# Performance work log

Measured on AMD Instinct MI355X. Metric: run time of the kernel, lower is better.

Reference implementation:

```python
import jax, jax.numpy as jnp
import numpy as np

DIM = 1024
HEADS = 8
NUM_EXPERTS = 65536
NUM_KEYS = 256  # sqrt(NUM_EXPERTS)
DIM_KEY = 512
TOPK = 16  # product_key_topk == num_experts_per_head


def setup_inputs() -> dict:
    key = jax.random.key(0)
    ks = jax.random.split(key, 6)
    B, N = 2, 512
    x = jax.random.normal(ks[0], (B, N, DIM), dtype=jnp.float32)
    gamma = jnp.ones((DIM,), dtype=jnp.float32)
    wq = jax.random.normal(ks[1], (2 * HEADS * DIM_KEY, DIM), dtype=jnp.float32) * 0.02
    keys = jax.random.normal(ks[2], (HEADS, NUM_KEYS, 2, DIM_KEY), dtype=jnp.float32) * 0.02
    table_down = jax.random.normal(ks[3], (NUM_EXPERTS, DIM), dtype=jnp.float32) * 0.02
    table_up = jax.random.normal(ks[4], (NUM_EXPERTS, DIM), dtype=jnp.float32) * 0.02
    return {"x": x, "gamma": gamma, "wq": wq, "keys": keys,
            "table_down": table_down, "table_up": table_up}


def _rmsnorm(v, g):
    # torch F.normalize(x, dim=-1) * gamma * sqrt(dim)
    scale = jnp.sqrt(jnp.asarray(v.shape[-1], v.dtype))
    n = jnp.maximum(jnp.linalg.norm(v, axis=-1, keepdims=True), 1e-12)
    return v / n * g * scale


def reference(x, gamma, wq, keys, table_down, table_up):
    B, N, D = x.shape
    xn = _rmsnorm(x, gamma)          # pre_rmsnorm on x
    gate = xn                        # x_in_gate is None -> gate = norm(x)
    # queries: b n (p h d) -> p b n h d
    q = gate @ wq.T                  # [B,N,2*H*DK]
    q = q.reshape(B, N, 2, HEADS, DIM_KEY).transpose(2, 0, 1, 3, 4)  # [2,B,N,H,DK]
    # sim: p b n h d, h k p d -> p b n h k
    sim = jnp.einsum('pbnhd,hkpd->pbnhk', q, keys)
    sx, ix = jax.lax.top_k(sim[0], TOPK)  # [B,N,H,TOPK]
    sy, iy = jax.lax.top_k(sim[1], TOPK)
    # outer sums over the two product-key axes -> [B,N,H,TOPK*TOPK]
    all_scores = (sx[..., :, None] + sy[..., None, :]).reshape(B, N, HEADS, TOPK * TOPK)
    all_indices = (ix[..., :, None] * NUM_KEYS + iy[..., None, :]).reshape(B, N, HEADS, TOPK * TOPK)
    scores, pk = jax.lax.top_k(all_scores, TOPK)           # [B,N,H,K]
    indices = jnp.take_along_axis(all_indices, pk, axis=-1)  # expert ids [B,N,H,K]
    wd = table_down[indices]  # [B,N,H,K,D]
    wu = table_up[indices]    # [B,N,H,K,D]
    h = jnp.einsum('bnd,bnhkd->bnhk', xn, wd)
    h = jax.nn.gelu(h, approximate=False) * jax.nn.softmax(scores, axis=-1)
    out = jnp.einsum('bnhk,bnhkd->bnd', h, wu)
    return out
```

## Files before the change

kernel.cpp:

```cpp
#include <hip/hip_runtime.h>
#include <math.h>


#define DIMV 1024

__global__ __launch_bounds__(256) void peer_rmsnorm(const float* __restrict__ x,
                                                    const float* __restrict__ gamma,
                                                    float* __restrict__ xnf)
{
    int t = blockIdx.x;
    int tid = threadIdx.x;
    const float4* xr = (const float4*)(x + (size_t)t * DIMV);
    float4 v = xr[tid];
    double ss = (double)v.x*v.x + (double)v.y*v.y + (double)v.z*v.z + (double)v.w*v.w;
    #pragma unroll
    for (int off = 32; off > 0; off >>= 1) ss += __shfl_xor(ss, off);
    __shared__ double red[4];
    if ((tid & 63) == 0) red[tid >> 6] = ss;
    __syncthreads();
    double tot = red[0] + red[1] + red[2] + red[3];
    float n32 = (float)fmax(sqrt(tot), 1e-12);
    const float4* g4 = (const float4*)gamma;
    float4 gv = g4[tid];
    float4 o;
    o.x = __fmul_rn(__fmul_rn(__fdiv_rn(v.x, n32), gv.x), 32.0f);
    o.y = __fmul_rn(__fmul_rn(__fdiv_rn(v.y, n32), gv.y), 32.0f);
    o.z = __fmul_rn(__fmul_rn(__fdiv_rn(v.z, n32), gv.z), 32.0f);
    o.w = __fmul_rn(__fmul_rn(__fdiv_rn(v.w, n32), gv.w), 32.0f);
    ((float4*)(xnf + (size_t)t * DIMV))[tid] = o;
}

__global__ __launch_bounds__(128) void peer_qgemm(const float* __restrict__ A,
                                                  const float* __restrict__ Bm,
                                                  float* __restrict__ C)
{
    __shared__ float As[2][16][128];
    __shared__ float Bs[2][16][128];
    int tid = threadIdx.x;
    int m0 = blockIdx.y * 128, n0 = blockIdx.x * 128;
    int tx = tid & 15, ty = tid >> 4;
    float acc[16][8] = {};
    float4 av0 = *(const float4*)(A  + (long)(m0 + tid) * 1024 + 0);
    float4 av1 = *(const float4*)(A  + (long)(m0 + tid) * 1024 + 4);
    float4 av2 = *(const float4*)(A  + (long)(m0 + tid) * 1024 + 8);
    float4 av3 = *(const float4*)(A  + (long)(m0 + tid) * 1024 + 12);
    float4 bv0 = *(const float4*)(Bm + (long)(n0 + tid) * 1024 + 0);
    float4 bv1 = *(const float4*)(Bm + (long)(n0 + tid) * 1024 + 4);
    float4 bv2 = *(const float4*)(Bm + (long)(n0 + tid) * 1024 + 8);
    float4 bv3 = *(const float4*)(Bm + (long)(n0 + tid) * 1024 + 12);
    #pragma unroll
    for (int j = 0; j < 4; j++) {
        As[0][j][tid]      = ((const float*)&av0)[j];
        As[0][4 + j][tid]  = ((const float*)&av1)[j];
        As[0][8 + j][tid]  = ((const float*)&av2)[j];
        As[0][12 + j][tid] = ((const float*)&av3)[j];
        Bs[0][j][tid]      = ((const float*)&bv0)[j];
        Bs[0][4 + j][tid]  = ((const float*)&bv1)[j];
        Bs[0][8 + j][tid]  = ((const float*)&bv2)[j];
        Bs[0][12 + j][tid] = ((const float*)&bv3)[j];
    }
    __syncthreads();
    int cur = 0;
    for (int k0 = 0; k0 < 1024; k0 += 16) {
        bool more = (k0 + 16) < 1024;
        if (more) {
            av0 = *(const float4*)(A  + (long)(m0 + tid) * 1024 + (k0 + 16));
            av1 = *(const float4*)(A  + (long)(m0 + tid) * 1024 + (k0 + 20));
            av2 = *(const float4*)(A  + (long)(m0 + tid) * 1024 + (k0 + 24));
            av3 = *(const float4*)(A  + (long)(m0 + tid) * 1024 + (k0 + 28));
            bv0 = *(const float4*)(Bm + (long)(n0 + tid) * 1024 + (k0 + 16));
            bv1 = *(const float4*)(Bm + (long)(n0 + tid) * 1024 + (k0 + 20));
            bv2 = *(const float4*)(Bm + (long)(n0 + tid) * 1024 + (k0 + 24));
            bv3 = *(const float4*)(Bm + (long)(n0 + tid) * 1024 + (k0 + 28));
        }
        #pragma unroll
        for (int kk = 0; kk < 16; kk++) {
            float4 a0 = *(const float4*)&As[cur][kk][ty * 16];
            float4 a1 = *(const float4*)&As[cur][kk][ty * 16 + 4];
            float4 a2 = *(const float4*)&As[cur][kk][ty * 16 + 8];
            float4 a3 = *(const float4*)&As[cur][kk][ty * 16 + 12];
            float4 b0 = *(const float4*)&Bs[cur][kk][tx * 4];
            float4 b1 = *(const float4*)&Bs[cur][kk][tx * 4 + 64];
            float ra16[16] = {a0.x,a0.y,a0.z,a0.w, a1.x,a1.y,a1.z,a1.w,
                              a2.x,a2.y,a2.z,a2.w, a3.x,a3.y,a3.z,a3.w};
            float rb8[8]   = {b0.x,b0.y,b0.z,b0.w, b1.x,b1.y,b1.z,b1.w};
            #pragma unroll
            for (int i = 0; i < 16; i++)
                #pragma unroll
                for (int j = 0; j < 8; j++)
                    acc[i][j] = __fmaf_rn(ra16[i], rb8[j], acc[i][j]);
        }
        if (more) {
            int nxt = cur ^ 1;
            #pragma unroll
            for (int j = 0; j < 4; j++) {
                As[nxt][j][tid]      = ((const float*)&av0)[j];
                As[nxt][4 + j][tid]  = ((const float*)&av1)[j];
                As[nxt][8 + j][tid]  = ((const float*)&av2)[j];
                As[nxt][12 + j][tid] = ((const float*)&av3)[j];
                Bs[nxt][j][tid]      = ((const float*)&bv0)[j];
                Bs[nxt][4 + j][tid]  = ((const float*)&bv1)[j];
                Bs[nxt][8 + j][tid]  = ((const float*)&bv2)[j];
                Bs[nxt][12 + j][tid] = ((const float*)&bv3)[j];
            }
            __syncthreads();
            cur = nxt;
        }
    }
    #pragma unroll
    for (int i = 0; i < 16; i++) {
        float4 c0 = {acc[i][0], acc[i][1], acc[i][2], acc[i][3]};
        float4 c1 = {acc[i][4], acc[i][5], acc[i][6], acc[i][7]};
        long r = (long)(m0 + ty * 16 + i) * 8192 + n0;
        *(float4*)(C + r + tx * 4)      = c0;
        *(float4*)(C + r + 64 + tx * 4) = c1;
    }
}

__global__ __launch_bounds__(256) void peer_sim(const float* __restrict__ qf,
                                                const float* __restrict__ keys,
                                                float* __restrict__ simf)
{
    int tb = blockIdx.x;
    int z  = blockIdx.y;
    int h = z & 7, p = z >> 3;
    int tid = threadIdx.x;
    __shared__ float4 qs[16][128];
    int t0 = tb * 16;
    long qbase = (long)h * 512 + (long)p * 4096;
    int row = tid >> 4, c0 = (tid & 15) * 8;
    const float4* qrow = (const float4*)(qf + (long)(t0 + row) * 8192 + qbase);
    #pragma unroll
    for (int u = 0; u < 8; u++) qs[row][c0 + u] = qrow[c0 + u];
    __syncthreads();
    int k = tid;
    const float4* krow = (const float4*)(keys + (long)h * 262144 + (long)k * 1024 + (long)p * 512);
    float pa[16][4] = {};
    for (int d4 = 0; d4 < 128; d4++) {
        float4 kv = krow[d4];
        #pragma unroll
        for (int tt = 0; tt < 16; tt++) {
            float4 qv = qs[tt][d4];
            pa[tt][0] = __fadd_rn(pa[tt][0], __fmul_rn(qv.x, kv.x));
            pa[tt][1] = __fadd_rn(pa[tt][1], __fmul_rn(qv.y, kv.y));
            pa[tt][2] = __fadd_rn(pa[tt][2], __fmul_rn(qv.z, kv.z));
            pa[tt][3] = __fadd_rn(pa[tt][3], __fmul_rn(qv.w, kv.w));
        }
    }
    #pragma unroll
    for (int tt = 0; tt < 16; tt++) {
        float s = __fadd_rn(__fadd_rn(pa[tt][0], pa[tt][2]),
                            __fadd_rn(pa[tt][1], pa[tt][3]));
        simf[(long)(t0 + tt) * 4096 + (long)p * 2048 + h * 256 + k] = s;
    }
}

__device__ inline void peer_select16(float v[4], int lane, float* outv, int* outi)
{
    for (int iter = 0; iter < 16; iter++) {
        float bv = -INFINITY; int bk = 1 << 30;
        #pragma unroll
        for (int i = 0; i < 4; i++) {
            int k = i * 64 + lane;
            if (v[i] > bv || (v[i] == bv && k < bk)) { bv = v[i]; bk = k; }
        }
        #pragma unroll
        for (int off = 32; off > 0; off >>= 1) {
            float ov = __shfl_xor(bv, off);
            int   ok = __shfl_xor(bk, off);
            if (ov > bv || (ov == bv && ok < bk)) { bv = ov; bk = ok; }
        }
        if (lane == 0) { outv[iter] = bv; outi[iter] = bk; }
        __syncthreads();
        if ((bk & 63) == lane) v[bk >> 6] = -INFINITY;
    }
}

__global__ __launch_bounds__(64) void peer_topk(const float* __restrict__ sim,
                                                float* __restrict__ wsel,
                                                int* __restrict__ esel)
{
    int b = blockIdx.x;
    int t = b >> 3, h = b & 7;
    int lane = threadIdx.x;
    const float* simx = sim + (size_t)t * 4096 + h * 256;
    const float* simy = simx + 2048;
    __shared__ float sxv[16]; __shared__ int sxi[16];
    __shared__ float syv[16]; __shared__ int syi[16];
    __shared__ float cv[16];  __shared__ int cf[16];
    float v[4];
    #pragma unroll
    for (int i = 0; i < 4; i++) v[i] = simx[i*64 + lane];
    peer_select16(v, lane, sxv, sxi);
    __syncthreads();
    #pragma unroll
    for (int i = 0; i < 4; i++) v[i] = simy[i*64 + lane];
    peer_select16(v, lane, syv, syi);
    __syncthreads();
    #pragma unroll
    for (int i = 0; i < 4; i++) {
        int f = i*64 + lane;
        v[i] = __fadd_rn(sxv[f >> 4], syv[f & 15]);
    }
    peer_select16(v, lane, cv, cf);
    __syncthreads();
    double m = (double)cv[0];
    double w = (lane < 16) ? exp((double)cv[lane] - m) : 0.0;
    double Z = w;
    #pragma unroll
    for (int off = 32; off > 0; off >>= 1) Z += __shfl_xor(Z, off);
    if (lane < 16) {
        int f = cf[lane];
        esel[b * 16 + lane] = sxi[f >> 4] * 256 + syi[f & 15];
        wsel[b * 16 + lane] = (float)(w / Z);
    }
}

__global__ __launch_bounds__(256) void peer_downup(const float* __restrict__ xn,
                                                   const float* __restrict__ table_down,
                                                   const float* __restrict__ table_up,
                                                   const int* __restrict__ esel,
                                                   const float* __restrict__ wsel,
                                                   float* __restrict__ out)
{
    int t = blockIdx.x;
    int tid = threadIdx.x;
    int wid = tid >> 6, lane = tid & 63;
    __shared__ float4 xs[256];
    __shared__ float  gs[128];
    __shared__ int    es[128];
    if (tid < 128) es[tid] = esel[t * 128 + tid];
    xs[tid] = ((const float4*)(xn + (size_t)t * DIMV))[tid];
    __syncthreads();
    #pragma unroll 4
    for (int jj = 0; jj < 32; jj++) {
        int j = wid * 32 + jj;
        const float4* dr = (const float4*)(table_down + (size_t)es[j] * DIMV);
        double acc = 0.0;
        #pragma unroll
        for (int it = 0; it < 4; it++) {
            int d4 = it * 64 + lane;
            float4 a = xs[d4];
            float4 bb = dr[d4];
            acc = fma((double)a.x, (double)bb.x, acc);
            acc = fma((double)a.y, (double)bb.y, acc);
            acc = fma((double)a.z, (double)bb.z, acc);
            acc = fma((double)a.w, (double)bb.w, acc);
        }
        #pragma unroll
        for (int off = 32; off > 0; off >>= 1) acc += __shfl_xor(acc, off);
        if (lane == 0) {
            double hv = acc;
            double ge = 0.5 * hv * (1.0 + erf(hv * 0.70710678118654752));
            gs[j] = (float)(ge * (double)wsel[t * 128 + j]);
        }
    }
    __syncthreads();
    int dbase = tid * 4;
    double a0 = 0, a1 = 0, a2 = 0, a3 = 0;
    #pragma unroll 8
    for (int j = 0; j < 128; j++) {
        const float4 u = *(const float4*)(table_up + (size_t)es[j] * DIMV + dbase);
        double gj = (double)gs[j];
        a0 = fma(gj, (double)u.x, a0); a1 = fma(gj, (double)u.y, a1);
        a2 = fma(gj, (double)u.z, a2); a3 = fma(gj, (double)u.w, a3);
    }
    float4 o = {(float)a0, (float)a1, (float)a2, (float)a3};
    *(float4*)(out + (size_t)t * DIMV + dbase) = o;
}

extern "C" void kernel_launch(void* const* d_in, const int* in_sizes, int n_in,
                              void* d_out, int out_size, void* d_ws, size_t ws_size,
                              hipStream_t stream)
{
    const float* x          = (const float*)d_in[0];
    const float* gamma      = (const float*)d_in[1];
    const float* wq         = (const float*)d_in[2];
    const float* keys       = (const float*)d_in[3];
    const float* table_down = (const float*)d_in[4];
    const float* table_up   = (const float*)d_in[5];
    float* out = (float*)d_out;
    char* wsb  = (char*)d_ws;

    float* xnf  = (float*)(wsb);
    float* qf   = (float*)(wsb + (4ull<<20));
    float* simf = (float*)(wsb + (36ull<<20));
    float* wsel = (float*)(wsb + (52ull<<20));
    int*   esel = (int*)  (wsb + (52ull<<20) + (512ull<<10));
    if (ws_size < (54ull << 20)) return;

    peer_rmsnorm<<<1024, 256, 0, stream>>>(x, gamma, xnf);

    peer_qgemm<<<dim3(64, 8, 1), 128, 0, stream>>>(xnf, wq, qf);

    peer_sim<<<dim3(64, 16, 1), 256, 0, stream>>>(qf, keys, simf);

    peer_topk<<<8192, 64, 0, stream>>>(simf, wsel, esel);

    peer_downup<<<1024, 256, 0, stream>>>(xnf, table_down, table_up,
                                          esel, wsel, out);
}
```

Before: 559.8 us.

## Shrink query GEMM tile to 128x64 and software-prefetch gathered table rows

The query GEMM tile drops from 128x128 to 128x64, doubling the grid to 1024 blocks. Each thread now holds an 8x8 accumulator instead of 16x8, which cuts register pressure and improves occupancy on the 256-CU GPU. In the down/up gather kernel, the next expert's table_down row and the next four table_up rows are loaded into registers before the current ones are used. This overlaps gather latency with the FP64 FMAs, at the cost of extra registers.

```diff
diff --git a/kernel.cpp b/kernel.cpp
--- a/kernel.cpp
+++ b/kernel.cpp
@@ -35,29 +35,26 @@
                                                   float* __restrict__ C)
 {
     __shared__ float As[2][16][128];
-    __shared__ float Bs[2][16][128];
+    __shared__ float Bs[2][16][64];
     int tid = threadIdx.x;
-    int m0 = blockIdx.y * 128, n0 = blockIdx.x * 128;
-    int tx = tid & 15, ty = tid >> 4;
-    float acc[16][8] = {};
+    int n0 = blockIdx.x * 64, m0 = blockIdx.y * 128;
+    int tx = tid & 7, ty = tid >> 3;
+    int rb = tid >> 1, lk8 = (tid & 1) * 8;
+    float acc[8][8] = {};
     float4 av0 = *(const float4*)(A  + (long)(m0 + tid) * 1024 + 0);
     float4 av1 = *(const float4*)(A  + (long)(m0 + tid) * 1024 + 4);
     float4 av2 = *(const float4*)(A  + (long)(m0 + tid) * 1024 + 8);
     float4 av3 = *(const float4*)(A  + (long)(m0 + tid) * 1024 + 12);
-    float4 bv0 = *(const float4*)(Bm + (long)(n0 + tid) * 1024 + 0);
-    float4 bv1 = *(const float4*)(Bm + (long)(n0 + tid) * 1024 + 4);
-    float4 bv2 = *(const float4*)(Bm + (long)(n0 + tid) * 1024 + 8);
-    float4 bv3 = *(const float4*)(Bm + (long)(n0 + tid) * 1024 + 12);
+    float4 bv0 = *(const float4*)(Bm + (long)(n0 + rb) * 1024 + lk8);
+    float4 bv1 = *(const float4*)(Bm + (long)(n0 + rb) * 1024 + lk8 + 4);
     #pragma unroll
     for (int j = 0; j < 4; j++) {
         As[0][j][tid]      = ((const float*)&av0)[j];
         As[0][4 + j][tid]  = ((const float*)&av1)[j];
         As[0][8 + j][tid]  = ((const float*)&av2)[j];
         As[0][12 + j][tid] = ((const float*)&av3)[j];
-        Bs[0][j][tid]      = ((const float*)&bv0)[j];
-        Bs[0][4 + j][tid]  = ((const float*)&bv1)[j];
-        Bs[0][8 + j][tid]  = ((const float*)&bv2)[j];
-        Bs[0][12 + j][tid] = ((const float*)&bv3)[j];
+        Bs[0][lk8 + j][rb]     = ((const float*)&bv0)[j];
+        Bs[0][lk8 + 4 + j][rb] = ((const float*)&bv1)[j];
     }
     __syncthreads();
     int cur = 0;
@@ -68,27 +65,22 @@
             av1 = *(const float4*)(A  + (long)(m0 + tid) * 1024 + (k0 + 20));
             av2 = *(const float4*)(A  + (long)(m0 + tid) * 1024 + (k0 + 24));
             av3 = *(const float4*)(A  + (long)(m0 + tid) * 1024 + (k0 + 28));
-            bv0 = *(const float4*)(Bm + (long)(n0 + tid) * 1024 + (k0 + 16));
-            bv1 = *(const float4*)(Bm + (long)(n0 + tid) * 1024 + (k0 + 20));
-            bv2 = *(const float4*)(Bm + (long)(n0 + tid) * 1024 + (k0 + 24));
-            bv3 = *(const float4*)(Bm + (long)(n0 + tid) * 1024 + (k0 + 28));
+            bv0 = *(const float4*)(Bm + (long)(n0 + rb) * 1024 + (k0 + 16 + lk8));
+            bv1 = *(const float4*)(Bm + (long)(n0 + rb) * 1024 + (k0 + 20 + lk8));
         }
         #pragma unroll
         for (int kk = 0; kk < 16; kk++) {
-            float4 a0 = *(const float4*)&As[cur][kk][ty * 16];
-            float4 a1 = *(const float4*)&As[cur][kk][ty * 16 + 4];
-            float4 a2 = *(const float4*)&As[cur][kk][ty * 16 + 8];
-            float4 a3 = *(const float4*)&As[cur][kk][ty * 16 + 12];
-            float4 b0 = *(const float4*)&Bs[cur][kk][tx * 4];
-            float4 b1 = *(const float4*)&Bs[cur][kk][tx * 4 + 64];
-            float ra16[16] = {a0.x,a0.y,a0.z,a0.w, a1.x,a1.y,a1.z,a1.w,
-                              a2.x,a2.y,a2.z,a2.w, a3.x,a3.y,a3.z,a3.w};
-            float rb8[8]   = {b0.x,b0.y,b0.z,b0.w, b1.x,b1.y,b1.z,b1.w};
+            float4 a0 = *(const float4*)&As[cur][kk][ty * 8];
+            float4 a1 = *(const float4*)&As[cur][kk][ty * 8 + 4];
+            float4 b0 = *(const float4*)&Bs[cur][kk][tx * 8];
+            float4 b1 = *(const float4*)&Bs[cur][kk][tx * 8 + 4];
+            float ra8[8] = {a0.x,a0.y,a0.z,a0.w, a1.x,a1.y,a1.z,a1.w};
+            float rb8[8] = {b0.x,b0.y,b0.z,b0.w, b1.x,b1.y,b1.z,b1.w};
             #pragma unroll
-            for (int i = 0; i < 16; i++)
+            for (int i = 0; i < 8; i++)
                 #pragma unroll
                 for (int j = 0; j < 8; j++)
-                    acc[i][j] = __fmaf_rn(ra16[i], rb8[j], acc[i][j]);
+                    acc[i][j] = __fmaf_rn(ra8[i], rb8[j], acc[i][j]);
         }
         if (more) {
             int nxt = cur ^ 1;
@@ -98,22 +90,20 @@
                 As[nxt][4 + j][tid]  = ((const float*)&av1)[j];
                 As[nxt][8 + j][tid]  = ((const float*)&av2)[j];
                 As[nxt][12 + j][tid] = ((const float*)&av3)[j];
-                Bs[nxt][j][tid]      = ((const float*)&bv0)[j];
-                Bs[nxt][4 + j][tid]  = ((const float*)&bv1)[j];
-                Bs[nxt][8 + j][tid]  = ((const float*)&bv2)[j];
-                Bs[nxt][12 + j][tid] = ((const float*)&bv3)[j];
+                Bs[nxt][lk8 + j][rb]     = ((const float*)&bv0)[j];
+                Bs[nxt][lk8 + 4 + j][rb] = ((const float*)&bv1)[j];
             }
             __syncthreads();
             cur = nxt;
         }
     }
     #pragma unroll
-    for (int i = 0; i < 16; i++) {
+    for (int i = 0; i < 8; i++) {
         float4 c0 = {acc[i][0], acc[i][1], acc[i][2], acc[i][3]};
         float4 c1 = {acc[i][4], acc[i][5], acc[i][6], acc[i][7]};
-        long r = (long)(m0 + ty * 16 + i) * 8192 + n0;
-        *(float4*)(C + r + tx * 4)      = c0;
-        *(float4*)(C + r + 64 + tx * 4) = c1;
+        long r = (long)(m0 + ty * 8 + i) * 8192 + (n0 + tx * 8);
+        *(float4*)(C + r)     = c0;
+        *(float4*)(C + r + 4) = c1;
     }
 }
 
@@ -232,40 +222,68 @@
     if (tid < 128) es[tid] = esel[t * 128 + tid];
     xs[tid] = ((const float4*)(xn + (size_t)t * DIMV))[tid];
     __syncthreads();
-    #pragma unroll 4
+    int base = wid * 32;
+    const float4* dr = (const float4*)(table_down + (size_t)es[base] * DIMV);
+    float4 p0 = dr[lane], p1 = dr[64 + lane], p2 = dr[128 + lane], p3 = dr[192 + lane];
+    float4 a0 = xs[lane], a1 = xs[64 + lane], a2 = xs[128 + lane], a3 = xs[192 + lane];
     for (int jj = 0; jj < 32; jj++) {
-        int j = wid * 32 + jj;
-        const float4* dr = (const float4*)(table_down + (size_t)es[j] * DIMV);
+        float4 c0 = p0, c1 = p1, c2 = p2, c3 = p3;
+        if (jj < 31) {
+            const float4* nr = (const float4*)(table_down + (size_t)es[base + jj + 1] * DIMV);
+            p0 = nr[lane]; p1 = nr[64 + lane]; p2 = nr[128 + lane]; p3 = nr[192 + lane];
+        }
         double acc = 0.0;
-        #pragma unroll
-        for (int it = 0; it < 4; it++) {
-            int d4 = it * 64 + lane;
-            float4 a = xs[d4];
-            float4 bb = dr[d4];
-            acc = fma((double)a.x, (double)bb.x, acc);
-            acc = fma((double)a.y, (double)bb.y, acc);
-            acc = fma((double)a.z, (double)bb.z, acc);
-            acc = fma((double)a.w, (double)bb.w, acc);
-        }
+        acc = fma((double)a0.x, (double)c0.x, acc);
+        acc = fma((double)a0.y, (double)c0.y, acc);
+        acc = fma((double)a0.z, (double)c0.z, acc);
+        acc = fma((double)a0.w, (double)c0.w, acc);
+        acc = fma((double)a1.x, (double)c1.x, acc);
+        acc = fma((double)a1.y, (double)c1.y, acc);
+        acc = fma((double)a1.z, (double)c1.z, acc);
+        acc = fma((double)a1.w, (double)c1.w, acc);
+        acc = fma((double)a2.x, (double)c2.x, acc);
+        acc = fma((double)a2.y, (double)c2.y, acc);
+        acc = fma((double)a2.z, (double)c2.z, acc);
+        acc = fma((double)a2.w, (double)c2.w, acc);
+        acc = fma((double)a3.x, (double)c3.x, acc);
+        acc = fma((double)a3.y, (double)c3.y, acc);
+        acc = fma((double)a3.z, (double)c3.z, acc);
+        acc = fma((double)a3.w, (double)c3.w, acc);
         #pragma unroll
         for (int off = 32; off > 0; off >>= 1) acc += __shfl_xor(acc, off);
         if (lane == 0) {
             double hv = acc;
             double ge = 0.5 * hv * (1.0 + erf(hv * 0.70710678118654752));
-            gs[j] = (float)(ge * (double)wsel[t * 128 + j]);
+            gs[base + jj] = (float)(ge * (double)wsel[t * 128 + base + jj]);
         }
     }
     __syncthreads();
     int dbase = tid * 4;
-    double a0 = 0, a1 = 0, a2 = 0, a3 = 0;
-    #pragma unroll 8
-    for (int j = 0; j < 128; j++) {
-        const float4 u = *(const float4*)(table_up + (size_t)es[j] * DIMV + dbase);
-        double gj = (double)gs[j];
-        a0 = fma(gj, (double)u.x, a0); a1 = fma(gj, (double)u.y, a1);
-        a2 = fma(gj, (double)u.z, a2); a3 = fma(gj, (double)u.w, a3);
-    }
-    float4 o = {(float)a0, (float)a1, (float)a2, (float)a3};
+    double b0 = 0, b1 = 0, b2 = 0, b3 = 0;
+    float4 u0 = *(const float4*)(table_up + (size_t)es[0] * DIMV + dbase);
+    float4 u1 = *(const float4*)(table_up + (size_t)es[1] * DIMV + dbase);
+    float4 u2 = *(const float4*)(table_up + (size_t)es[2] * DIMV + dbase);
+    float4 u3 = *(const float4*)(table_up + (size_t)es[3] * DIMV + dbase);
+    for (int j = 0; j < 128; j += 4) {
+        float4 c0 = u0, c1 = u1, c2 = u2, c3 = u3;
+        if (j + 4 < 128) {
+            u0 = *(const float4*)(table_up + (size_t)es[j + 4] * DIMV + dbase);
+            u1 = *(const float4*)(table_up + (size_t)es[j + 5] * DIMV + dbase);
+            u2 = *(const float4*)(table_up + (size_t)es[j + 6] * DIMV + dbase);
+            u3 = *(const float4*)(table_up + (size_t)es[j + 7] * DIMV + dbase);
+        }
+        double g0 = (double)gs[j],     g1 = (double)gs[j + 1];
+        double g2 = (double)gs[j + 2], g3 = (double)gs[j + 3];
+        b0 = fma(g0, (double)c0.x, b0); b1 = fma(g0, (double)c0.y, b1);
+        b2 = fma(g0, (double)c0.z, b2); b3 = fma(g0, (double)c0.w, b3);
+        b0 = fma(g1, (double)c1.x, b0); b1 = fma(g1, (double)c1.y, b1);
+        b2 = fma(g1, (double)c1.z, b2); b3 = fma(g1, (double)c1.w, b3);
+        b0 = fma(g2, (double)c2.x, b0); b1 = fma(g2, (double)c2.y, b1);
+        b2 = fma(g2, (double)c2.z, b2); b3 = fma(g2, (double)c2.w, b3);
+        b0 = fma(g3, (double)c3.x, b0); b1 = fma(g3, (double)c3.y, b1);
+        b2 = fma(g3, (double)c3.z, b2); b3 = fma(g3, (double)c3.w, b3);
+    }
+    float4 o = {(float)b0, (float)b1, (float)b2, (float)b3};
     *(float4*)(out + (size_t)t * DIMV + dbase) = o;
 }
 
@@ -291,7 +309,7 @@
 
     peer_rmsnorm<<<1024, 256, 0, stream>>>(x, gamma, xnf);
 
-    peer_qgemm<<<dim3(64, 8, 1), 128, 0, stream>>>(xnf, wq, qf);
+    peer_qgemm<<<dim3(128, 8, 1), 128, 0, stream>>>(xnf, wq, qf);
 
     peer_sim<<<dim3(64, 16, 1), 256, 0, stream>>>(qf, keys, simf);
 
```

Result: no change. 570.0 us (+1.8%).
